# Kernel optimization log

Measured on AMD Instinct MI355X. Metric: run time of the kernel, lower is better.

## Reference

```python
import jax, jax.numpy as jnp
import numpy as np

B, D, H, E, W, R = 2048, 1024, 2048, 16, 4, 8
SCALE = 1.0


def setup_inputs() -> dict:
    key = jax.random.key(0)
    ks = jax.random.split(key, 10)
    s = 0.02
    return dict(
        z=jax.random.normal(ks[0], (B, D), jnp.float32),
        top_k=2,
        capacity=256,
        ban_expert=-1,
        tau=jnp.float32(1.0),
        epsilon=jnp.float32(0.0),
        fc1_w=jax.random.uniform(ks[1], (H, D), jnp.float32, -1.0, 1.0) / np.sqrt(D),
        fc1_b=jnp.zeros((H,), jnp.float32),
        fc2_w=jax.random.uniform(ks[2], (D, H), jnp.float32, -1.0, 1.0) / np.sqrt(H),
        fc2_b=jnp.zeros((D,), jnp.float32),
        prototypes=s * jax.random.normal(ks[3], (E, D), jnp.float32),
        adapter_keys=s * jax.random.normal(ks[4], (E, W, D), jnp.float32),
        expert_bias=jnp.zeros((E,), jnp.float32),
        a1=s * jax.random.normal(ks[5], (E, W, R, D), jnp.float32),
        b1=s * jax.random.normal(ks[6], (E, W, H, R), jnp.float32),
        a2=s * jax.random.normal(ks[7], (E, W, R, H), jnp.float32),
        b2=s * jax.random.normal(ks[8], (E, W, D, R), jnp.float32),
    )


def capacity_route(probs, top_k, capacity):
    # Greedy, order-dependent capacity-limited top-k routing (faithful to the
    # Python double loop): tokens processed in order, each takes its highest-
    # prob candidates whose expert still has free capacity.
    Bn, En = probs.shape
    k = min(top_k, En)
    cand_k = min(En, max(4 * k, k))
    cap_limit = max(1, capacity)
    vals, idxs = jax.lax.top_k(probs, cand_k)  # [B, cand_k]

    def token_step(cap, row):
        v_row, i_row = row

        def cand_step(st, x):
            slot, cap, a_idx, a_w, hit = st
            v, e, j = x
            take = (slot < k) & (cap[e] < cap_limit)
            s = jnp.minimum(slot, k - 1)
            a_idx = a_idx.at[s].set(jnp.where(take, e, a_idx[s]))
            a_w = a_w.at[s].set(jnp.where(take, v, a_w[s]))
            cap = cap.at[e].add(jnp.where(take, 1, 0).astype(cap.dtype))
            hit = hit + jnp.where(take & (j > 0), 1, 0)
            slot = slot + jnp.where(take, 1, 0)
            return (slot, cap, a_idx, a_w, hit), None

        init = (jnp.int32(0), cap,
                jnp.full((k,), -1, jnp.int32),
                jnp.zeros((k,), probs.dtype),
                jnp.int32(0))
        (slot, cap, a_idx, a_w, hit), _ = jax.lax.scan(
            cand_step, init, (v_row, i_row.astype(jnp.int32), jnp.arange(cand_k)))
        return cap, (a_idx, a_w, hit)

    cap0 = jnp.zeros((En,), jnp.int32)
    _, (assigned_idx, assigned_w, hits) = jax.lax.scan(token_step, cap0, (vals, idxs))
    cap_hit_rate = hits.sum().astype(probs.dtype) / max(1, Bn * k)
    return assigned_idx, assigned_w, cap_hit_rate


def reference(z, top_k, capacity, ban_expert, tau, epsilon,
              fc1_w, fc1_b, fc2_w, fc2_b, prototypes, adapter_keys,
              expert_bias, a1, b1, a2, b2):
    Bn = z.shape[0]
    En = prototypes.shape[0]
    h_pre = jax.nn.silu(z @ fc1_w.T + fc1_b)          # [B, H]
    out_pre = h_pre @ fc2_w.T + fc2_b                 # [B, D]

    logits = (z @ prototypes.T) / jnp.maximum(tau, 1e-6) + expert_bias
    logits = jnp.where(jnp.arange(En)[None, :] == ban_expert, -1e9, logits)
    probs = jax.nn.softmax(logits, axis=-1)
    probs = (1.0 - epsilon) * probs + epsilon / En

    assigned_idx, assigned_w, cap_hit_rate = capacity_route(probs, top_k, capacity)
    k = assigned_idx.shape[1]
    valid = assigned_idx >= 0                          # [B, k]
    e_safe = jnp.where(valid, assigned_idx, 0)         # [B, k]

    # adapter selection: argmax_w  z . adapter_keys[e, w]
    ak = adapter_keys[e_safe]                          # [B, k, W, D]
    a_idx = jnp.argmax(jnp.einsum('bd,bkwd->bkw', z, ak), axis=-1)  # [B, k]

    A1 = a1[e_safe, a_idx]                             # [B, k, R, D]
    B1 = b1[e_safe, a_idx]                             # [B, k, H, R]
    A2 = a2[e_safe, a_idx]                             # [B, k, R, H]
    B2 = b2[e_safe, a_idx]                             # [B, k, D, R]

    t1 = jnp.einsum('bd,bkrd->bkr', z, A1)
    d1 = jnp.einsum('bkr,bkhr->bkh', t1, B1) * SCALE
    h = jax.nn.silu(h_pre[:, None, :] + d1)            # [B, k, H]
    t2 = jnp.einsum('bkh,bkrh->bkr', h, A2)
    d2 = jnp.einsum('bkr,bkdr->bkd', t2, B2) * SCALE
    y = out_pre[:, None, :] + d2                       # [B, k, D]

    w = jnp.where(valid, assigned_w, 0.0)[:, :, None].astype(z.dtype)
    z_out = (w * y).sum(axis=1)                        # [B, D]

    used_mask = jnp.zeros((Bn, En), bool).at[jnp.arange(Bn)[:, None], e_safe].max(valid)
    # event lists, slot-major order, -1 marks unassigned slots (fixed shape for jit)
    ev_e = jnp.where(valid, assigned_idx, -1).T.reshape(-1)
    ev_a = jnp.where(valid, a_idx, -1).T.reshape(-1)

    return (z + z_out, probs, used_mask, assigned_idx, assigned_w,
            cap_hit_rate, ev_e, ev_a)
```

## Files before the change

kernel.cpp:

```cpp
#include <hip/hip_runtime.h>
#include <stdint.h>

#define NTOK 2048
#define DDIM 1024
#define HDIM 2048
#define NEXP 16

#define O_PROBS 2097152
#define O_USED  2129920
#define O_AIDX  2162688
#define O_AW    2166784
#define O_HIT   2170880
#define O_EVE   2170881
#define O_EVA   2174977

static constexpr size_t WS_ZBF    = 0;
static constexpr size_t WS_FC1WBF = WS_ZBF    + (size_t)NTOK * DDIM * 2;
static constexpr size_t WS_FC2WBF = WS_FC1WBF + (size_t)HDIM * DDIM * 2;
static constexpr size_t WS_HPREBF = WS_FC2WBF + (size_t)DDIM * HDIM * 2;
static constexpr size_t WS_OUTPRE = WS_HPREBF + (size_t)NTOK * HDIM * 2;
static constexpr size_t WS_A1BF   = WS_OUTPRE + (size_t)NTOK * DDIM * 4;
static constexpr size_t WS_B1BF   = WS_A1BF   + (size_t)16 * 4 * 8 * 1024 * 2;
static constexpr size_t WS_A2BF   = WS_B1BF   + (size_t)16 * 4 * 2048 * 8 * 2;
static constexpr size_t WS_B2BF   = WS_A2BF   + (size_t)16 * 4 * 8 * 2048 * 2;
static constexpr size_t WS_CANDS  = WS_B2BF   + (size_t)16 * 4 * 1024 * 8 * 2;
static constexpr size_t WS_CVALS  = WS_CANDS  + (size_t)NTOK * 4;
static constexpr size_t WS_ARGPK  = WS_CVALS  + (size_t)NTOK * 8 * 4;
static constexpr size_t WS_ASGN   = WS_ARGPK  + (size_t)NTOK * 4;
static constexpr size_t WS_ASGNW  = WS_ASGN   + (size_t)NTOK * 4;
static constexpr size_t WS_OUTPR2 = WS_ASGNW  + (size_t)NTOK * 2 * 4;
static constexpr size_t WS_TOTAL2 = WS_OUTPR2 + (size_t)NTOK * DDIM * 4;

typedef __bf16 v8bf __attribute__((ext_vector_type(8)));
typedef float v4f __attribute__((ext_vector_type(4)));
typedef unsigned short us8v __attribute__((ext_vector_type(8)));

__device__ __forceinline__ unsigned short f2bf(float f) {
  unsigned u = __float_as_uint(f);
  u = u + 0x7fffu + ((u >> 16) & 1u);
  return (unsigned short)(u >> 16);
}
__device__ __forceinline__ float bf2f(unsigned short s) {
  return __uint_as_float(((unsigned)s) << 16);
}
__device__ __forceinline__ void gload_lds16(const void* g, void* l) {
  __builtin_amdgcn_global_load_lds(
      (const __attribute__((address_space(1))) void*)g,
      (__attribute__((address_space(3))) void*)l, 16, 0, 0);
}
__device__ __forceinline__ float dot4(float4 a, float4 b) {
  return a.x * b.x + a.y * b.y + a.z * b.z + a.w * b.w;
}

__global__ __launch_bounds__(256) void k1_scores(
    const float* __restrict__ z, const float* __restrict__ proto,
    const float* __restrict__ ebias, const float* __restrict__ ak,
    const float* __restrict__ p_tau, const float* __restrict__ p_eps,
    const int* __restrict__ p_ban,
    unsigned short* __restrict__ zbf, float* __restrict__ out,
    unsigned* __restrict__ cands, float* __restrict__ cvals,
    unsigned* __restrict__ argpk)
{
  __shared__ float zs[4][DDIM];
  __shared__ float part[80 * 17];
  __shared__ float sc[4 * 80];
  const int tid = threadIdx.x;
  const int tb = blockIdx.x * 4;
#pragma unroll
  for (int i = 0; i < 4; ++i) {
    const int col = tid * 4;
    float4 v = *(const float4*)&z[(size_t)(tb + i) * DDIM + col];
    *(float4*)&zs[i][col] = v;
    ushort4 bv;
    bv.x = f2bf(v.x); bv.y = f2bf(v.y); bv.z = f2bf(v.z); bv.w = f2bf(v.w);
    *(ushort4*)&zbf[(size_t)(tb + i) * DDIM + col] = bv;
  }
  __syncthreads();
  const int wv = tid >> 6, l = tid & 63;

  {
    const float4* akr = (const float4*)(ak + (size_t)l * DDIM + wv * 256);
    const float4* z0 = (const float4*)&zs[0][0] + wv * 64;
    const float4* z1 = (const float4*)&zs[1][0] + wv * 64;
    const float4* z2 = (const float4*)&zs[2][0] + wv * 64;
    const float4* z3 = (const float4*)&zs[3][0] + wv * 64;
    float a0 = 0.f, a1v = 0.f, a2v = 0.f, a3 = 0.f;
#pragma unroll 8
    for (int i = 0; i < 64; ++i) {
      float4 w = akr[i];
      a0 += dot4(z0[i], w); a1v += dot4(z1[i], w);
      a2v += dot4(z2[i], w); a3 += dot4(z3[i], w);
    }
    part[l * 17 + 0 * 4 + wv] = a0;
    part[l * 17 + 1 * 4 + wv] = a1v;
    part[l * 17 + 2 * 4 + wv] = a2v;
    part[l * 17 + 3 * 4 + wv] = a3;
  }
  if (l < 16) {
    const float4* pr = (const float4*)(proto + (size_t)l * DDIM + wv * 256);
    const float4* z0 = (const float4*)&zs[0][0] + wv * 64;
    const float4* z1 = (const float4*)&zs[1][0] + wv * 64;
    const float4* z2 = (const float4*)&zs[2][0] + wv * 64;
    const float4* z3 = (const float4*)&zs[3][0] + wv * 64;
    float a0 = 0.f, a1v = 0.f, a2v = 0.f, a3 = 0.f;
#pragma unroll 8
    for (int i = 0; i < 64; ++i) {
      float4 w = pr[i];
      a0 += dot4(z0[i], w); a1v += dot4(z1[i], w);
      a2v += dot4(z2[i], w); a3 += dot4(z3[i], w);
    }
    part[(64 + l) * 17 + 0 * 4 + wv] = a0;
    part[(64 + l) * 17 + 1 * 4 + wv] = a1v;
    part[(64 + l) * 17 + 2 * 4 + wv] = a2v;
    part[(64 + l) * 17 + 3 * 4 + wv] = a3;
  }
  __syncthreads();
  for (int o = tid; o < 320; o += 256) {
    const int row = o >> 2, tk = o & 3;
    sc[tk * 80 + row] =
        ((part[row * 17 + tk * 4 + 0] + part[row * 17 + tk * 4 + 1]) +
         part[row * 17 + tk * 4 + 2]) + part[row * 17 + tk * 4 + 3];
  }
  __syncthreads();
  if (tid < 4) {
    const int t = tb + tid;
    const float tau = fmaxf(p_tau[0], 1e-6f);
    const float eps = p_eps[0];
    const int ban = p_ban[0];
    float lg[16];
#pragma unroll
    for (int e = 0; e < 16; ++e) {
      float v = sc[tid * 80 + 64 + e] / tau + ebias[e];
      lg[e] = (e == ban) ? -1e9f : v;
    }
    float mx = lg[0];
#pragma unroll
    for (int e = 1; e < 16; ++e) mx = fmaxf(mx, lg[e]);
    float ex[16]; float sm = 0.f;
#pragma unroll
    for (int e = 0; e < 16; ++e) { ex[e] = expf(lg[e] - mx); sm += ex[e]; }
    float p[16];
#pragma unroll
    for (int e = 0; e < 16; ++e) {
      p[e] = (1.f - eps) * (ex[e] / sm) + eps / (float)NEXP;
      out[O_PROBS + (size_t)t * NEXP + e] = p[e];
    }
    unsigned pack = 0, taken = 0;
#pragma unroll
    for (int r = 0; r < 8; ++r) {
      float bv = -1e30f; int bi = 0;
#pragma unroll
      for (int e = 0; e < 16; ++e) {
        const bool c = !((taken >> e) & 1u) && (p[e] > bv);
        bv = c ? p[e] : bv; bi = c ? e : bi;
      }
      taken |= 1u << bi;
      pack |= ((unsigned)bi) << (4 * r);
      cvals[(size_t)t * 8 + r] = bv;
    }
    cands[t] = pack;
    unsigned apk = 0;
#pragma unroll
    for (int e = 0; e < 16; ++e) {
      float b = sc[tid * 80 + e * 4]; int bi = 0;
#pragma unroll
      for (int w = 1; w < 4; ++w) {
        const float v = sc[tid * 80 + e * 4 + w];
        if (v > b) { b = v; bi = w; }
      }
      apk |= ((unsigned)bi) << (2 * e);
    }
    argpk[t] = apk;
  }
}

#define CONVB 224

__device__ __forceinline__ void route_decide(unsigned c, int avail,
                                             unsigned& m, int& dec) {
  unsigned flags = 0;
#pragma unroll
  for (int j = 0; j < 8; ++j) {
    const int e = (c >> (4 * j)) & 15;
    flags |= ((unsigned)(avail >> e) & 1u) << j;
  }
  const int pc = __popc(flags);
  const int sc = pc < 2 ? pc : 2;
  const int j0 = __ffs(flags) - 1;
  const int j1 = __ffs(flags & (flags - 1)) - 1;
  const int r0 = sc > 0 ? j0 : 0;
  const int r1 = sc > 1 ? j1 : 0;
  const int e0 = (c >> (4 * r0)) & 15;
  const int e1 = (c >> (4 * r1)) & 15;
  m = (sc > 0 ? (1u << e0) : 0u) | (sc > 1 ? (1u << e1) : 0u);
  dec = e0 | (e1 << 4) | (r0 << 8) | (r1 << 11) | (sc << 14);
}

__global__ __launch_bounds__(1024) void k2_route_conv(
    const unsigned* __restrict__ cands, const float* __restrict__ cvals,
    const unsigned* __restrict__ argpk, const int* __restrict__ p_cap,
    float* __restrict__ out, int* __restrict__ asgn, float* __restrict__ asgnw,
    const float* __restrict__ fc1w, const float* __restrict__ fc2w,
    const float* __restrict__ a1, const float* __restrict__ b1,
    const float* __restrict__ a2, const float* __restrict__ b2,
    unsigned short* __restrict__ fc1wbf, unsigned short* __restrict__ fc2wbf,
    unsigned short* __restrict__ a1bf, unsigned short* __restrict__ b1bf,
    unsigned short* __restrict__ a2bf, unsigned short* __restrict__ b2bf)
{
  const int tid = threadIdx.x;
  if (blockIdx.x != 0) {
    size_t j = (size_t)(blockIdx.x - 1) * 1024 + tid;
    const size_t stride = (size_t)CONVB * 1024;
    for (; j < 1835008ull; j += stride) {
      const float* src; unsigned short* dst; size_t off;
      if (j < 524288) { src = fc1w; dst = fc1wbf; off = j; }
      else if (j < 1048576) { src = fc2w; dst = fc2wbf; off = j - 524288; }
      else if (j < 1179648) { src = a1; dst = a1bf; off = j - 1048576; }
      else if (j < 1441792) { src = b1; dst = b1bf; off = j - 1179648; }
      else if (j < 1703936) { src = a2; dst = a2bf; off = j - 1441792; }
      else { src = b2; dst = b2bf; off = j - 1703936; }
      float4 v = *(const float4*)&src[off * 4];
      ushort4 bv;
      bv.x = f2bf(v.x); bv.y = f2bf(v.y); bv.z = f2bf(v.z); bv.w = f2bf(v.w);
      *(ushort4*)&dst[off * 4] = bv;
    }
    return;
  }
  __shared__ unsigned long long bal[2][32][17];
  __shared__ int T[16];
  __shared__ int hitsS;
  const int w = tid >> 6, l = tid & 63;
  if (tid == 0) hitsS = 0;
  const int capl = max(1, p_cap[0]);
  const unsigned cA = cands[tid], cB = cands[tid + 1024];
  const unsigned aA = argpk[tid], aB = argpk[tid + 1024];
  float cvA[8], cvB[8];
#pragma unroll
  for (int q = 0; q < 8; ++q) {
    cvA[q] = cvals[(size_t)tid * 8 + q];
    cvB[q] = cvals[(size_t)(tid + 1024) * 8 + q];
  }
  int avail = 0xFFFF, t0 = 0, capw = 0, hits = 0;

  for (int round = 0; round < 20; ++round) {
    const int p = round & 1;
    unsigned mA = 0, mB = 0;
    int dA = 0, dB = 0;
    if (tid >= t0) route_decide(cA, avail, mA, dA);
    if (tid + 1024 >= t0) route_decide(cB, avail, mB, dB);
    if (w * 64 + 63 >= t0) {
      for (int av = avail; av; av &= av - 1) {
        const int e = __ffs(av) - 1;
        unsigned long long b = __ballot((mA >> e) & 1);
        if (l == e) bal[p][w][l] = b;
      }
    } else if (l < 16) {
      bal[p][w][l] = 0ull;
    }
    {
      for (int av = avail; av; av &= av - 1) {
        const int e = __ffs(av) - 1;
        unsigned long long b = __ballot((mB >> e) & 1);
        if (l == e) bal[p][w + 16][l] = b;
      }
    }
    __syncthreads();
    unsigned long long bm = 0;
    int myT = 0x7FFFFFFF;
    const bool eav = (avail >> w) & 1;
    if (eav) {
      int cnt = 0;
      if (l < 32) { bm = bal[p][l][w]; cnt = __popcll(bm); }
      int tot = cnt;
#pragma unroll
      for (int o = 32; o; o >>= 1) tot += __shfl_xor(tot, o, 64);
      const int rem = capl - capw;
      if (tot >= rem) {
        int incl = cnt;
#pragma unroll
        for (int o = 1; o < 32; o <<= 1) {
          int u = __shfl_up(incl, o, 64);
          if (l >= o) incl += u;
        }
        if (l < 32) {
          const int need = rem - (incl - cnt);
          if (need >= 1 && need <= cnt) {
            unsigned long long bb = bm;
            for (int i = 1; i < need; ++i) bb &= bb - 1;
            myT = l * 64 + (__ffsll((unsigned long long)bb) - 1);
          }
        }
#pragma unroll
        for (int o = 32; o; o >>= 1) myT = min(myT, __shfl_xor(myT, o, 64));
      }
    }
    if (l == 0) T[w] = myT;
    __syncthreads();
    const int tv = (l < 16) ? T[l] : 0x7FFFFFFF;
    int ts = tv;
#pragma unroll
    for (int o = 32; o; o >>= 1) ts = min(ts, __shfl_xor(ts, o, 64));
    const bool done = (ts == 0x7FFFFFFF);
    const int tfin = done ? (NTOK - 1) : ts;
    unsigned long long crossed = __ballot((l < 16) && !done && (tv == ts));
    if (eav) {
      int c2 = 0;
      if (l < 32) {
        const int hi = tfin - l * 64;
        unsigned long long mk =
            (hi < 0) ? 0ull : (hi >= 63 ? ~0ull : ((1ull << (hi + 1)) - 1ull));
        c2 = __popcll(bm & mk);
      }
#pragma unroll
      for (int o = 32; o; o >>= 1) c2 += __shfl_xor(c2, o, 64);
      capw += c2;
    }
    {
      const int t = tid;
      if (t >= t0 && t <= tfin) {
        const int e0 = dA & 15, e1 = (dA >> 4) & 15;
        const int r0 = (dA >> 8) & 7, r1 = (dA >> 11) & 7, sc = (dA >> 14) & 3;
        const int a0 = (aA >> (2 * e0)) & 3, a1i = (aA >> (2 * e1)) & 3;
        float w0 = 0.f, w1v = 0.f;
#pragma unroll
        for (int q = 0; q < 8; ++q) {
          if (q == r0) w0 = cvA[q];
          if (q == r1) w1v = cvA[q];
        }
        asgn[t] = e0 | (e1 << 4) | (a0 << 8) | (a1i << 10) | (sc << 12);
        asgnw[t * 2 + 0] = sc > 0 ? w0 : 0.f;
        asgnw[t * 2 + 1] = sc > 1 ? w1v : 0.f;
        hits += (sc > 0 && r0 > 0) + (sc > 1 && r1 > 0);
      }
    }
    {
      const int t = tid + 1024;
      if (t >= t0 && t <= tfin) {
        const int e0 = dB & 15, e1 = (dB >> 4) & 15;
        const int r0 = (dB >> 8) & 7, r1 = (dB >> 11) & 7, sc = (dB >> 14) & 3;
        const int a0 = (aB >> (2 * e0)) & 3, a1i = (aB >> (2 * e1)) & 3;
        float w0 = 0.f, w1v = 0.f;
#pragma unroll
        for (int q = 0; q < 8; ++q) {
          if (q == r0) w0 = cvB[q];
          if (q == r1) w1v = cvB[q];
        }
        asgn[t] = e0 | (e1 << 4) | (a0 << 8) | (a1i << 10) | (sc << 12);
        asgnw[t * 2 + 0] = sc > 0 ? w0 : 0.f;
        asgnw[t * 2 + 1] = sc > 1 ? w1v : 0.f;
        hits += (sc > 0 && r0 > 0) + (sc > 1 && r1 > 0);
      }
    }
    avail &= ~(int)(unsigned)(crossed & 0xFFFFull);
    t0 = tfin + 1;
    if (done) break;
  }
#pragma unroll
  for (int o = 32; o; o >>= 1) hits += __shfl_xor(hits, o, 64);
  if (l == 0) atomicAdd(&hitsS, hits);
  __syncthreads();
  if (tid == 0) out[O_HIT] = (float)hitsS / (float)(NTOK * 2);
}

template <int EPI>
__device__ __forceinline__ void gemm_body(
    unsigned short* As, unsigned short* Bs, int bid,
    const unsigned short* __restrict__ A, const unsigned short* __restrict__ Bm,
    const float* __restrict__ bias, void* __restrict__ Cout,
    int M, int N, int Kloop, int lda, int add_bias)
{
  const int tid = threadIdx.x;
  const int wv = tid >> 6, l = tid & 63;
  const int ntile = N >> 7;
  const int trow = (bid / ntile) << 7;
  const int tcol = (bid % ntile) << 7;
  const int wr = wv >> 1, wc = wv & 1;
  v4f acc[4][4];
#pragma unroll
  for (int m = 0; m < 4; ++m)
#pragma unroll
    for (int n = 0; n < 4; ++n) acc[m][n] = (v4f){0.f, 0.f, 0.f, 0.f};

  const int lrow8 = l >> 3;
  const int lcol8 = (l & 7) << 3;
  const unsigned short* gA = A + (size_t)trow * lda;
  const unsigned short* gB = Bm + (size_t)tcol * lda;
  const int fr = l & 15, kof = (l >> 4) << 3;

  for (int k0 = 0; k0 < Kloop; k0 += 64) {
    __syncthreads();
#pragma unroll
    for (int i = 0; i < 4; ++i) {
      const int s = (wv << 2) + i;
      gload_lds16(gA + (size_t)(s * 8 + lrow8) * lda + k0 + lcol8, &As[s * 512]);
      gload_lds16(gB + (size_t)(s * 8 + lrow8) * lda + k0 + lcol8, &Bs[s * 512]);
    }
    __syncthreads();
    v8bf af[4][2], bf[4][2];
#pragma unroll
    for (int m = 0; m < 4; ++m) {
      const int row = wr * 64 + m * 16 + fr;
      af[m][0] = *(const v8bf*)&As[row * 64 + kof];
      af[m][1] = *(const v8bf*)&As[row * 64 + 32 + kof];
    }
#pragma unroll
    for (int n = 0; n < 4; ++n) {
      const int row = wc * 64 + n * 16 + fr;
      bf[n][0] = *(const v8bf*)&Bs[row * 64 + kof];
      bf[n][1] = *(const v8bf*)&Bs[row * 64 + 32 + kof];
    }
#pragma unroll
    for (int ks = 0; ks < 2; ++ks)
#pragma unroll
      for (int m = 0; m < 4; ++m)
#pragma unroll
        for (int n = 0; n < 4; ++n)
          acc[m][n] = __builtin_amdgcn_mfma_f32_16x16x32_bf16(
              af[m][ks], bf[n][ks], acc[m][n], 0, 0, 0);
  }
  const int fq = l >> 4;
#pragma unroll
  for (int m = 0; m < 4; ++m)
#pragma unroll
    for (int n = 0; n < 4; ++n) {
      const int col = tcol + wc * 64 + n * 16 + fr;
      const float bc = add_bias ? bias[col] : 0.f;
#pragma unroll
      for (int j = 0; j < 4; ++j) {
        const int row = trow + wr * 64 + m * 16 + fq * 4 + j;
        const float v = acc[m][n][j] + bc;
        if (EPI == 0) {
          const float sv = v / (1.f + __expf(-v));
          ((unsigned short*)Cout)[(size_t)row * N + col] = f2bf(sv);
        } else {
          ((float*)Cout)[(size_t)row * N + col] = v;
        }
      }
    }
}

__global__ __launch_bounds__(256) void gemm_bt0(
    const unsigned short* __restrict__ A, const unsigned short* __restrict__ Bm,
    const float* __restrict__ bias, void* __restrict__ Cout,
    int M, int N, int K)
{
  __shared__ __align__(16) char smem[32768];
  gemm_body<0>((unsigned short*)smem, (unsigned short*)smem + 8192,
               blockIdx.x, A, Bm, bias, Cout, M, N, K, K, 1);
}

__global__ __launch_bounds__(256) void gemm_bt1s(
    const unsigned short* __restrict__ A, const unsigned short* __restrict__ Bm,
    const float* __restrict__ bias, float* __restrict__ C0,
    float* __restrict__ C1)
{
  __shared__ __align__(16) char smem[32768];
  const int ntiles = (NTOK / 128) * (DDIM / 128);
  const int half = blockIdx.x / ntiles;
  const int tile = blockIdx.x % ntiles;
  gemm_body<1>((unsigned short*)smem, (unsigned short*)smem + 8192,
               tile, A + half * 1024, Bm + half * 1024, bias,
               half ? (void*)C1 : (void*)C0,
               NTOK, DDIM, 1024, HDIM, half == 0);
}

__global__ __launch_bounds__(256) void gemm_bt1f(
    const unsigned short* __restrict__ A, const unsigned short* __restrict__ Bm,
    const float* __restrict__ bias, void* __restrict__ Cout,
    int M, int N, int K)
{
  __shared__ __align__(16) char smem[32768];
  gemm_body<1>((unsigned short*)smem, (unsigned short*)smem + 8192,
               blockIdx.x, A, Bm, bias, Cout, M, N, K, K, 1);
}

__global__ __launch_bounds__(256) void k5_lora(
    const float* __restrict__ z, const unsigned short* __restrict__ hpre,
    const float* __restrict__ outpre, const float* __restrict__ outpre2,
    int use2, const int* __restrict__ asgn, const float* __restrict__ asgnw,
    const unsigned short* __restrict__ a1, const unsigned short* __restrict__ b1,
    const unsigned short* __restrict__ a2, const unsigned short* __restrict__ b2,
    float* __restrict__ out0, float* __restrict__ out)
{
  __shared__ float zl[DDIM];
  __shared__ float hl[2][HDIM];
  __shared__ float d2a[2][DDIM];
  __shared__ float t1s[2][8], t2s[2][8];
  const int b = blockIdx.x, tid = threadIdx.x;
  {
    float4 v = *(const float4*)&z[(size_t)b * DDIM + tid * 4];
    *(float4*)&zl[tid * 4] = v;
  }
#pragma unroll
  for (int j = 0; j < 8; ++j) ((float*)d2a)[tid + 256 * j] = 0.f;
  const int pk = asgn[b];
  const int sc = (pk >> 12) & 3;
  const int eA0 = pk & 15, eA1 = (pk >> 4) & 15;
  const int aA0 = (pk >> 8) & 3, aA1 = (pk >> 10) & 3;
  const float w0 = asgnw[b * 2 + 0], w1 = asgnw[b * 2 + 1];
  if (tid < 16)
    out[O_USED + (size_t)b * 16 + tid] =
        (float)((sc > 0 && tid == eA0) || (sc > 1 && tid == eA1));
  if (tid == 0) {
    out[O_AIDX + (size_t)b * 2 + 0] = sc > 0 ? (float)eA0 : -1.f;
    out[O_AIDX + (size_t)b * 2 + 1] = sc > 1 ? (float)eA1 : -1.f;
    out[O_AW + (size_t)b * 2 + 0] = w0;
    out[O_AW + (size_t)b * 2 + 1] = w1;
    out[O_EVE + b] = sc > 0 ? (float)eA0 : -1.f;
    out[O_EVE + NTOK + b] = sc > 1 ? (float)eA1 : -1.f;
    out[O_EVA + b] = sc > 0 ? (float)aA0 : -1.f;
    out[O_EVA + NTOK + b] = sc > 1 ? (float)aA1 : -1.f;
  }
  const int half = tid >> 7;
  const int ht = tid & 127;
  const int r4 = ht >> 5, l5 = ht & 31;
  const bool valid = half < sc;
  const float ww = half ? w1 : w0;
  const int ad = (half ? eA1 : eA0) * 4 + (half ? aA1 : aA0);
  const float4* zg = (const float4*)&z[(size_t)b * DDIM];
  __syncthreads();

  if (valid) {
#pragma unroll
    for (int rr = r4; rr < 8; rr += 4) {
      const us8v* pa1 = (const us8v*)(a1 + ((size_t)ad * 8 + rr) * DDIM);
      float sa = 0.f;
#pragma unroll
      for (int i = 0; i < 4; ++i) {
        const int g = l5 + 32 * i;
        us8v va = pa1[g];
        float4 z0 = zg[g * 2], z1 = zg[g * 2 + 1];
        sa += z0.x * bf2f(va[0]) + z0.y * bf2f(va[1]) +
              z0.z * bf2f(va[2]) + z0.w * bf2f(va[3]) +
              z1.x * bf2f(va[4]) + z1.y * bf2f(va[5]) +
              z1.z * bf2f(va[6]) + z1.w * bf2f(va[7]);
      }
#pragma unroll
      for (int o = 16; o; o >>= 1) sa += __shfl_xor(sa, o, 64);
      if (l5 == 0) t1s[half][rr] = sa;
    }
  }
  __syncthreads();
  if (valid) {
    float t1r[8];
#pragma unroll
    for (int q = 0; q < 8; ++q) t1r[q] = t1s[half][q];
    const unsigned short* pb1 = b1 + (size_t)ad * HDIM * 8;
    const unsigned short* ph = hpre + (size_t)b * HDIM;
#pragma unroll
    for (int j = 0; j < 16; ++j) {
      const int hh_i = ht + 128 * j;
      us8v row = *(const us8v*)&pb1[(size_t)hh_i * 8];
      float d1 = 0.f;
#pragma unroll
      for (int q = 0; q < 8; ++q) d1 += t1r[q] * bf2f(row[q]);
      const float hh = bf2f(ph[hh_i]) + d1;
      hl[half][hh_i] = hh / (1.f + __expf(-hh));
    }
  }
  __syncthreads();
  if (valid) {
#pragma unroll
    for (int rr = r4; rr < 8; rr += 4) {
      const us8v* pa2 = (const us8v*)(a2 + ((size_t)ad * 8 + rr) * HDIM);
      float sa = 0.f;
#pragma unroll
      for (int i = 0; i < 8; ++i) {
        const int g = l5 + 32 * i;
        us8v va = pa2[g];
        const float* hp = &hl[half][g * 8];
        sa += hp[0] * bf2f(va[0]) + hp[1] * bf2f(va[1]) +
              hp[2] * bf2f(va[2]) + hp[3] * bf2f(va[3]) +
              hp[4] * bf2f(va[4]) + hp[5] * bf2f(va[5]) +
              hp[6] * bf2f(va[6]) + hp[7] * bf2f(va[7]);
      }
#pragma unroll
      for (int o = 16; o; o >>= 1) sa += __shfl_xor(sa, o, 64);
      if (l5 == 0) t2s[half][rr] = sa;
    }
  }
  __syncthreads();
  if (valid) {
    float t2r[8];
#pragma unroll
    for (int q = 0; q < 8; ++q) t2r[q] = t2s[half][q];
    const unsigned short* pb2 = b2 + (size_t)ad * DDIM * 8;
#pragma unroll
    for (int j = 0; j < 8; ++j) {
      const int d = ht + 128 * j;
      us8v row = *(const us8v*)&pb2[(size_t)d * 8];
      float d2 = 0.f;
#pragma unroll
      for (int q = 0; q < 8; ++q) d2 += t2r[q] * bf2f(row[q]);
      d2a[half][d] = ww * d2;
    }
  }
  __syncthreads();
  const float wsum = (sc > 0 ? w0 : 0.f) + (sc > 1 ? w1 : 0.f);
#pragma unroll
  for (int j = 0; j < 4; ++j) {
    const int d = tid + 256 * j;
    float op = outpre[(size_t)b * DDIM + d];
    if (use2) op += outpre2[(size_t)b * DDIM + d];
    out0[(size_t)b * DDIM + d] = zl[d] + wsum * op + d2a[0][d] + d2a[1][d];
  }
}

extern "C" void kernel_launch(void* const* d_in, const int* in_sizes, int n_in,
                              void* d_out, int out_size, void* d_ws, size_t ws_size,
                              hipStream_t stream)
{
  (void)in_sizes; (void)n_in; (void)out_size;
  const float* z     = (const float*)d_in[0];
  const int*   p_cap = (const int*)d_in[2];
  const int*   p_ban = (const int*)d_in[3];
  const float* p_tau = (const float*)d_in[4];
  const float* p_eps = (const float*)d_in[5];
  const float* fc1w  = (const float*)d_in[6];
  const float* fc1b  = (const float*)d_in[7];
  const float* fc2w  = (const float*)d_in[8];
  const float* fc2b  = (const float*)d_in[9];
  const float* proto = (const float*)d_in[10];
  const float* ak    = (const float*)d_in[11];
  const float* ebias = (const float*)d_in[12];
  const float* a1    = (const float*)d_in[13];
  const float* b1    = (const float*)d_in[14];
  const float* a2    = (const float*)d_in[15];
  const float* b2    = (const float*)d_in[16];
  float* out = (float*)d_out;
  char* ws = (char*)d_ws;

  unsigned short* zbf    = (unsigned short*)(ws + WS_ZBF);
  unsigned short* fc1wbf = (unsigned short*)(ws + WS_FC1WBF);
  unsigned short* fc2wbf = (unsigned short*)(ws + WS_FC2WBF);
  unsigned short* hprebf = (unsigned short*)(ws + WS_HPREBF);
  float*          outpre = (float*)(ws + WS_OUTPRE);
  unsigned short* a1bf   = (unsigned short*)(ws + WS_A1BF);
  unsigned short* b1bf   = (unsigned short*)(ws + WS_B1BF);
  unsigned short* a2bf   = (unsigned short*)(ws + WS_A2BF);
  unsigned short* b2bf   = (unsigned short*)(ws + WS_B2BF);
  unsigned*       cands  = (unsigned*)(ws + WS_CANDS);
  float*          cvals  = (float*)(ws + WS_CVALS);
  unsigned*       argpk  = (unsigned*)(ws + WS_ARGPK);
  int*            asgn   = (int*)(ws + WS_ASGN);
  float*          asgnw  = (float*)(ws + WS_ASGNW);
  float*          outpr2 = (float*)(ws + WS_OUTPR2);
  const int splitk = (ws_size >= WS_TOTAL2) ? 1 : 0;

  k1_scores<<<512, 256, 0, stream>>>(
      z, proto, ebias, ak, p_tau, p_eps, p_ban, zbf, out, cands, cvals, argpk);

  k2_route_conv<<<1 + CONVB, 1024, 0, stream>>>(
      cands, cvals, argpk, p_cap, out, asgn, asgnw,
      fc1w, fc2w, a1, b1, a2, b2,
      fc1wbf, fc2wbf, a1bf, b1bf, a2bf, b2bf);

  gemm_bt0<<<(NTOK / 128) * (HDIM / 128), 256, 0, stream>>>(
      zbf, fc1wbf, fc1b, (void*)hprebf, NTOK, HDIM, DDIM);

  if (splitk) {
    gemm_bt1s<<<2 * (NTOK / 128) * (DDIM / 128), 256, 0, stream>>>(
        hprebf, fc2wbf, fc2b, outpre, outpr2);
  } else {
    gemm_bt1f<<<(NTOK / 128) * (DDIM / 128), 256, 0, stream>>>(
        hprebf, fc2wbf, fc2b, (void*)outpre, NTOK, DDIM, HDIM);
  }

  k5_lora<<<NTOK, 256, 0, stream>>>(
      z, hprebf, outpre, outpr2, splitk, asgn, asgnw,
      a1bf, b1bf, a2bf, b2bf, out, out);
}
```

Baseline: 259.8 us.

## Fuse fc1 GEMM into routing kernel so it overlaps serial routing

Moves the fc1 weight bf16 conversion into the scores kernel. The standalone fc1 GEMM launch is replaced by 128 extra blocks in the routing kernel, running a new 1024-thread 256x128-tile MFMA GEMM. Those blocks run concurrently with the single-block sequential capacity router and the remaining weight conversions. The aim is to hide the long serial routing phase behind the large GEMM and to save one launch. The cost is a less tuned GEMM: big 1024-thread blocks, a single LDS buffer and a barrier on every k step.

```diff
diff --git a/kernel.cpp b/kernel.cpp
--- a/kernel.cpp
+++ b/kernel.cpp
@@ -59,7 +59,8 @@
     const int* __restrict__ p_ban,
     unsigned short* __restrict__ zbf, float* __restrict__ out,
     unsigned* __restrict__ cands, float* __restrict__ cvals,
-    unsigned* __restrict__ argpk)
+    unsigned* __restrict__ argpk,
+    const float* __restrict__ fc1w, unsigned short* __restrict__ fc1wbf)
 {
   __shared__ float zs[4][DDIM];
   __shared__ float part[80 * 17];
@@ -172,9 +173,93 @@
     }
     argpk[t] = apk;
   }
-}
-
-#define CONVB 224
+  {
+    size_t j = (size_t)blockIdx.x * 256 + tid;
+    for (; j < 524288ull; j += (size_t)512 * 256) {
+      float4 v = *(const float4*)&fc1w[j * 4];
+      ushort4 bv;
+      bv.x = f2bf(v.x); bv.y = f2bf(v.y); bv.z = f2bf(v.z); bv.w = f2bf(v.w);
+      *(ushort4*)&fc1wbf[j * 4] = bv;
+    }
+  }
+}
+
+template <int EPI>
+__device__ __forceinline__ void gemm_w16(
+    unsigned short* As, unsigned short* Bs, int bid,
+    const unsigned short* __restrict__ A, const unsigned short* __restrict__ Bm,
+    const float* __restrict__ bias, void* __restrict__ Cout,
+    int N, int Kloop, int lda, int add_bias)
+{
+  const int tid = threadIdx.x;
+  const int wv = tid >> 6, l = tid & 63;
+  const int ntile = N >> 7;
+  const int trow = (bid / ntile) << 8;
+  const int tcol = (bid % ntile) << 7;
+  const int wr = wv >> 1, wc = wv & 1;
+  v4f acc[2][4];
+#pragma unroll
+  for (int m = 0; m < 2; ++m)
+#pragma unroll
+    for (int n = 0; n < 4; ++n) acc[m][n] = (v4f){0.f, 0.f, 0.f, 0.f};
+
+  const int lrow8 = l >> 3;
+  const int lcol8 = (l & 7) << 3;
+  const unsigned short* gA = A + (size_t)trow * lda;
+  const unsigned short* gB = Bm + (size_t)tcol * lda;
+  const int fr = l & 15, kof = (l >> 4) << 3;
+
+  for (int k0 = 0; k0 < Kloop; k0 += 64) {
+    __syncthreads();
+#pragma unroll
+    for (int i = 0; i < 2; ++i) {
+      const int s = wv * 2 + i;
+      gload_lds16(gA + (size_t)(s * 8 + lrow8) * lda + k0 + lcol8, &As[s * 512]);
+    }
+    gload_lds16(gB + (size_t)(wv * 8 + lrow8) * lda + k0 + lcol8, &Bs[wv * 512]);
+    __syncthreads();
+    v8bf af[2][2], bf[4][2];
+#pragma unroll
+    for (int m = 0; m < 2; ++m) {
+      const int row = wr * 32 + m * 16 + fr;
+      af[m][0] = *(const v8bf*)&As[row * 64 + kof];
+      af[m][1] = *(const v8bf*)&As[row * 64 + 32 + kof];
+    }
+#pragma unroll
+    for (int n = 0; n < 4; ++n) {
+      const int row = wc * 64 + n * 16 + fr;
+      bf[n][0] = *(const v8bf*)&Bs[row * 64 + kof];
+      bf[n][1] = *(const v8bf*)&Bs[row * 64 + 32 + kof];
+    }
+#pragma unroll
+    for (int ks = 0; ks < 2; ++ks)
+#pragma unroll
+      for (int m = 0; m < 2; ++m)
+#pragma unroll
+        for (int n = 0; n < 4; ++n)
+          acc[m][n] = __builtin_amdgcn_mfma_f32_16x16x32_bf16(
+              af[m][ks], bf[n][ks], acc[m][n], 0, 0, 0);
+  }
+  const int fq = l >> 4;
+#pragma unroll
+  for (int m = 0; m < 2; ++m)
+#pragma unroll
+    for (int n = 0; n < 4; ++n) {
+      const int col = tcol + wc * 64 + n * 16 + fr;
+      const float bc = add_bias ? bias[col] : 0.f;
+#pragma unroll
+      for (int j = 0; j < 4; ++j) {
+        const int row = trow + wr * 32 + m * 16 + fq * 4 + j;
+        const float v = acc[m][n][j] + bc;
+        if (EPI == 0) {
+          const float sv = v / (1.f + __expf(-v));
+          ((unsigned short*)Cout)[(size_t)row * N + col] = f2bf(sv);
+        } else {
+          ((float*)Cout)[(size_t)row * N + col] = v;
+        }
+      }
+    }
+}
 
 __device__ __forceinline__ void route_decide(unsigned c, int avail,
                                              unsigned& m, int& dec) {
@@ -196,29 +281,37 @@
   dec = e0 | (e1 << 4) | (r0 << 8) | (r1 << 11) | (sc << 14);
 }
 
-__global__ __launch_bounds__(1024) void k2_route_conv(
+__global__ __launch_bounds__(1024, 1) void k2_fc1_route_conv(
+    const unsigned short* __restrict__ Azbf,
+    const unsigned short* __restrict__ Bfc1wbf,
+    const float* __restrict__ fc1b, unsigned short* __restrict__ hprebf,
     const unsigned* __restrict__ cands, const float* __restrict__ cvals,
     const unsigned* __restrict__ argpk, const int* __restrict__ p_cap,
     float* __restrict__ out, int* __restrict__ asgn, float* __restrict__ asgnw,
-    const float* __restrict__ fc1w, const float* __restrict__ fc2w,
+    const float* __restrict__ fc2w,
     const float* __restrict__ a1, const float* __restrict__ b1,
     const float* __restrict__ a2, const float* __restrict__ b2,
-    unsigned short* __restrict__ fc1wbf, unsigned short* __restrict__ fc2wbf,
+    unsigned short* __restrict__ fc2wbf,
     unsigned short* __restrict__ a1bf, unsigned short* __restrict__ b1bf,
     unsigned short* __restrict__ a2bf, unsigned short* __restrict__ b2bf)
 {
+  __shared__ __align__(16) unsigned short As[256 * 64];
+  __shared__ __align__(16) unsigned short Bs[128 * 64];
+  __shared__ unsigned long long bal[2][32][17];
+  __shared__ int T[16];
+  __shared__ int hitsS;
   const int tid = threadIdx.x;
-  if (blockIdx.x != 0) {
-    size_t j = (size_t)(blockIdx.x - 1) * 1024 + tid;
-    const size_t stride = (size_t)CONVB * 1024;
-    for (; j < 1835008ull; j += stride) {
+
+  if (blockIdx.x >= 129) {
+    size_t j = (size_t)(blockIdx.x - 129) * 1024 + tid;
+    const size_t stride = (size_t)64 * 1024;
+    for (; j < 1310720ull; j += stride) {
       const float* src; unsigned short* dst; size_t off;
-      if (j < 524288) { src = fc1w; dst = fc1wbf; off = j; }
-      else if (j < 1048576) { src = fc2w; dst = fc2wbf; off = j - 524288; }
-      else if (j < 1179648) { src = a1; dst = a1bf; off = j - 1048576; }
-      else if (j < 1441792) { src = b1; dst = b1bf; off = j - 1179648; }
-      else if (j < 1703936) { src = a2; dst = a2bf; off = j - 1441792; }
-      else { src = b2; dst = b2bf; off = j - 1703936; }
+      if (j < 524288) { src = fc2w; dst = fc2wbf; off = j; }
+      else if (j < 655360) { src = a1; dst = a1bf; off = j - 524288; }
+      else if (j < 917504) { src = b1; dst = b1bf; off = j - 655360; }
+      else if (j < 1179648) { src = a2; dst = a2bf; off = j - 917504; }
+      else { src = b2; dst = b2bf; off = j - 1179648; }
       float4 v = *(const float4*)&src[off * 4];
       ushort4 bv;
       bv.x = f2bf(v.x); bv.y = f2bf(v.y); bv.z = f2bf(v.z); bv.w = f2bf(v.w);
@@ -226,9 +319,11 @@
     }
     return;
   }
-  __shared__ unsigned long long bal[2][32][17];
-  __shared__ int T[16];
-  __shared__ int hitsS;
+  if (blockIdx.x >= 1) {
+    gemm_w16<0>(As, Bs, blockIdx.x - 1, Azbf, Bfc1wbf, fc1b, (void*)hprebf,
+                HDIM, DDIM, DDIM, 1);
+    return;
+  }
   const int w = tid >> 6, l = tid & 63;
   if (tid == 0) hitsS = 0;
   const int capl = max(1, p_cap[0]);
@@ -437,16 +532,6 @@
         }
       }
     }
-}
-
-__global__ __launch_bounds__(256) void gemm_bt0(
-    const unsigned short* __restrict__ A, const unsigned short* __restrict__ Bm,
-    const float* __restrict__ bias, void* __restrict__ Cout,
-    int M, int N, int K)
-{
-  __shared__ __align__(16) char smem[32768];
-  gemm_body<0>((unsigned short*)smem, (unsigned short*)smem + 8192,
-               blockIdx.x, A, Bm, bias, Cout, M, N, K, K, 1);
 }
 
 __global__ __launch_bounds__(256) void gemm_bt1s(
@@ -648,15 +733,13 @@
   const int splitk = (ws_size >= WS_TOTAL2) ? 1 : 0;
 
   k1_scores<<<512, 256, 0, stream>>>(
-      z, proto, ebias, ak, p_tau, p_eps, p_ban, zbf, out, cands, cvals, argpk);
-
-  k2_route_conv<<<1 + CONVB, 1024, 0, stream>>>(
+      z, proto, ebias, ak, p_tau, p_eps, p_ban, zbf, out, cands, cvals, argpk,
+      fc1w, fc1wbf);
+
+  k2_fc1_route_conv<<<193, 1024, 0, stream>>>(
+      zbf, fc1wbf, fc1b, hprebf,
       cands, cvals, argpk, p_cap, out, asgn, asgnw,
-      fc1w, fc2w, a1, b1, a2, b2,
-      fc1wbf, fc2wbf, a1bf, b1bf, a2bf, b2bf);
-
-  gemm_bt0<<<(NTOK / 128) * (HDIM / 128), 256, 0, stream>>>(
-      zbf, fc1wbf, fc1b, (void*)hprebf, NTOK, HDIM, DDIM);
+      fc2w, a1, b1, a2, b2, fc2wbf, a1bf, b1bf, a2bf, b2bf);
 
   if (splitk) {
     gemm_bt1s<<<2 * (NTOK / 128) * (DDIM / 128), 256, 0, stream>>>(
```

Result: faster. 235.5 us (-9.4%).
